# Performance work log

Measured on AMD Instinct MI355X. Metric: run time of the kernel, lower is better.

Reference implementation:

```python
import jax, jax.numpy as jnp
import numpy as np

N_GRAPHS = 256
N_NODES = 100000
N_EDGES = 1000000
EMB = 64
EMB_RBF = 16
NUM_HEADS = 1


def setup_inputs() -> dict:
    key = jax.random.key(0)
    ks = jax.random.split(key, 10)
    edge_emb = jax.random.normal(ks[0], (N_EDGES, EMB), dtype=jnp.float32)
    edge_index = jax.random.randint(ks[1], (2, N_EDGES), 0, N_NODES, dtype=jnp.int64)
    distance_vec = jax.random.normal(ks[2], (N_EDGES, 3), dtype=jnp.float32)
    lattice = jax.random.normal(ks[3], (N_GRAPHS, 3, 3), dtype=jnp.float32)
    batch = jnp.sort(jax.random.randint(ks[4], (N_NODES,), 0, N_GRAPHS, dtype=jnp.int64))
    rbf = jax.random.uniform(ks[5], (N_EDGES, EMB_RBF), dtype=jnp.float32)
    # Dense layers (GemNet Dense defaults to bias=False)
    s = 1.0 / np.sqrt(EMB)
    W1 = jax.random.normal(ks[6], (EMB, EMB), dtype=jnp.float32) * s
    W2 = jax.random.normal(ks[7], (EMB, EMB), dtype=jnp.float32) * s
    W_rbf = jax.random.normal(ks[8], (EMB_RBF, EMB), dtype=jnp.float32) * (1.0 / np.sqrt(EMB_RBF))
    W_out = jax.random.normal(ks[9], (EMB, NUM_HEADS), dtype=jnp.float32) * s
    return {"edge_emb": edge_emb, "edge_index": edge_index, "distance_vec": distance_vec,
            "lattice": lattice, "batch": batch, "rbf": rbf,
            "W1": W1, "W2": W2, "W_rbf": W_rbf, "W_out": W_out}


def reference(edge_emb, edge_index, distance_vec, lattice, batch, rbf, W1, W2, W_rbf, W_out):
    # compute_score_per_edge: MLP on edge embeddings, gated by RBF projection
    h = jax.nn.silu(edge_emb @ W1)            # [E, EMB]
    x_F = h @ W2                               # [E, EMB]
    x_F = x_F * (rbf @ W_rbf)                  # RBF gate, [E, EMB]
    edge_scores = x_F @ W_out                  # [E, num_heads]

    batch_edge = batch[edge_index[0]]          # graph id per edge, [E]
    # normalize_score=True: divide by edge count per graph
    num_edges = jax.ops.segment_sum(jnp.ones((edge_scores.shape[0],), dtype=edge_scores.dtype),
                                    batch_edge, num_segments=N_GRAPHS)
    edge_scores = edge_scores / num_edges[batch_edge, None]

    # edge_score_to_lattice_score_frac_symmetric, summed over heads (num_heads=1)
    s = edge_scores[:, 0]                      # [E]
    unit = distance_vec / jnp.linalg.norm(distance_vec, axis=-1, keepdims=True)
    outer = s[:, None, None] * unit[:, :, None] * distance_vec[:, None, :]  # [E,3,3]
    sym = 0.5 * (outer + jnp.swapaxes(outer, 1, 2))
    out = jax.ops.segment_sum(sym, batch_edge, num_segments=N_GRAPHS)       # [B,3,3]
    return out
```

## Files before the change

kernel.cpp:

```cpp
#include <hip/hip_runtime.h>
#include <math.h>

constexpr int G    = 256;
constexpr int EMB  = 64;
constexpr int ERBF = 16;

typedef __attribute__((ext_vector_type(8))) short bf16x8;
typedef __attribute__((ext_vector_type(4))) float f32x4;

static __device__ __forceinline__ short bf16_rne(float f) {
    union { float f; unsigned u; } v; v.f = f;
    unsigned r = (v.u + 0x7FFFu + ((v.u >> 16) & 1u)) >> 16;
    return (short)r;
}

__global__ void prep_M_kernel(const float* __restrict__ W2,
                              const float* __restrict__ W_rbf,
                              const float* __restrict__ W_out,
                              float* __restrict__ M) {
    int t = blockIdx.x * blockDim.x + threadIdx.x;
    if (t >= EMB * ERBF) return;
    int p = t >> 4;
    int k = t & 15;
    float acc = 0.f;
    for (int j = 0; j < EMB; ++j)
        acc = fmaf(W2[p * EMB + j] * W_out[j], W_rbf[k * EMB + j], acc);
    M[p * ERBF + k] = acc;
}

__global__ __launch_bounds__(256, 4) void edge_kernel(
    const float* __restrict__ edge_emb,
    const int*   __restrict__ edge_src,
    const float* __restrict__ dvec,
    const int*   __restrict__ batch,
    const float* __restrict__ rbf,
    const float* __restrict__ W1,
    const float* __restrict__ M,
    float* __restrict__ partial,
    int ne, int nblk)
{
    __shared__ float accs[G * 9];

    const int tid  = threadIdx.x;
    const int w    = tid >> 6;
    const int lane = tid & 63;
    const int q    = lane >> 4;
    const int col  = lane & 15;

    for (int i = tid; i < G * 9; i += 256) accs[i] = 0.f;

    bf16x8 w1f[4][2];
#pragma unroll
    for (int nt = 0; nt < 4; ++nt)
#pragma unroll
        for (int c = 0; c < 2; ++c) {
            bf16x8 wv;
#pragma unroll
            for (int j = 0; j < 8; ++j)
                wv[j] = bf16_rne(W1[(c * 32 + q * 8 + j) * EMB + nt * 16 + col]);
            w1f[nt][c] = wv;
        }
    bf16x8 mtf[4];
#pragma unroll
    for (int nt = 0; nt < 4; ++nt) {
        bf16x8 mv;
#pragma unroll
        for (int j = 0; j < 8; ++j) {
            int k = q * 8 + j;
            mv[j] = (k < ERBF) ? bf16_rne(M[(nt * 16 + col) * ERBF + k]) : (short)0;
        }
        mtf[nt] = mv;
    }
    __syncthreads();

    const long estep = (long)nblk * 4 * 16;
    for (long e0 = ((long)blockIdx.x * 4 + w) * 16; e0 < ne; e0 += estep) {
        const long erow  = e0 + col;
        const bool rowok = (erow < ne);

        bf16x8 af[2];
#pragma unroll
        for (int c = 0; c < 2; ++c) {
            bf16x8 a;
            if (rowok) {
                const float4* p = (const float4*)(edge_emb + (size_t)erow * EMB + c * 32 + q * 8);
                float4 v0 = p[0], v1 = p[1];
                a[0] = bf16_rne(v0.x); a[1] = bf16_rne(v0.y);
                a[2] = bf16_rne(v0.z); a[3] = bf16_rne(v0.w);
                a[4] = bf16_rne(v1.x); a[5] = bf16_rne(v1.y);
                a[6] = bf16_rne(v1.z); a[7] = bf16_rne(v1.w);
            } else {
#pragma unroll
                for (int j = 0; j < 8; ++j) a[j] = 0;
            }
            af[c] = a;
        }
        bf16x8 rf;
        if (q < 2 && rowok) {
            const float4* p = (const float4*)(rbf + (size_t)erow * ERBF + q * 8);
            float4 v0 = p[0], v1 = p[1];
            rf[0] = bf16_rne(v0.x); rf[1] = bf16_rne(v0.y);
            rf[2] = bf16_rne(v0.z); rf[3] = bf16_rne(v0.w);
            rf[4] = bf16_rne(v1.x); rf[5] = bf16_rne(v1.y);
            rf[6] = bf16_rne(v1.z); rf[7] = bf16_rne(v1.w);
        } else {
#pragma unroll
            for (int j = 0; j < 8; ++j) rf[j] = 0;
        }

        f32x4 hacc[4], vacc[4];
#pragma unroll
        for (int nt = 0; nt < 4; ++nt) {
            f32x4 z = {0.f, 0.f, 0.f, 0.f};
            z = __builtin_amdgcn_mfma_f32_16x16x32_bf16(af[0], w1f[nt][0], z, 0, 0, 0);
            z = __builtin_amdgcn_mfma_f32_16x16x32_bf16(af[1], w1f[nt][1], z, 0, 0, 0);
            hacc[nt] = z;
            f32x4 zv = {0.f, 0.f, 0.f, 0.f};
            vacc[nt] = __builtin_amdgcn_mfma_f32_16x16x32_bf16(rf, mtf[nt], zv, 0, 0, 0);
        }

        float sc[4];
#pragma unroll
        for (int r = 0; r < 4; ++r) {
            float acc = 0.f;
#pragma unroll
            for (int nt = 0; nt < 4; ++nt) {
                float x = hacc[nt][r];
                float s = x * __builtin_amdgcn_rcpf(1.f + __expf(-x));
                acc = fmaf(s, vacc[nt][r], acc);
            }
            sc[r] = acc;
        }
#pragma unroll
        for (int m = 1; m < 16; m <<= 1) {
#pragma unroll
            for (int r = 0; r < 4; ++r) sc[r] += __shfl_xor(sc[r], m);
        }

        if (col < 4) {
            long e = e0 + q * 4 + col;
            if (e < ne) {
                float s = sc[col];
                int   g = batch[edge_src[e]];
                size_t de = (size_t)e * 3;
                float dx = dvec[de], dy = dvec[de + 1], dz = dvec[de + 2];
                float nrm = sqrtf(dx * dx + dy * dy + dz * dz);
                float cc = s / nrm;
                float* a = &accs[g * 9];
                atomicAdd(a + 0, cc * dx * dx);
                atomicAdd(a + 1, cc * dx * dy);
                atomicAdd(a + 2, cc * dx * dz);
                atomicAdd(a + 3, cc * dy * dy);
                atomicAdd(a + 4, cc * dy * dz);
                atomicAdd(a + 5, cc * dz * dz);
                atomicAdd(a + 6, 1.0f);
            }
        }
    }

    __syncthreads();
    float* outp = partial + (size_t)blockIdx.x * (G * 8);
    {
        int g = tid;
        float* a = &accs[g * 9];
        float4 p0 = {a[0], a[1], a[2], a[3]};
        float4 p1 = {a[4], a[5], a[6], 0.f};
        ((float4*)(outp + g * 8))[0] = p0;
        ((float4*)(outp + g * 8))[1] = p1;
    }
}

__global__ __launch_bounds__(256) void reduce_kernel(
    const float* __restrict__ partial, float* __restrict__ out, int nblk)
{
    int g = blockIdx.x;
    __shared__ float red[256][8];
    float loc[8];
#pragma unroll
    for (int c = 0; c < 8; ++c) loc[c] = 0.f;

    for (int b = threadIdx.x; b < nblk; b += 256) {
        const float4* p = (const float4*)(partial + (size_t)b * (G * 8) + g * 8);
        float4 v0 = p[0], v1 = p[1];
        loc[0] += v0.x; loc[1] += v0.y; loc[2] += v0.z; loc[3] += v0.w;
        loc[4] += v1.x; loc[5] += v1.y; loc[6] += v1.z; loc[7] += v1.w;
    }
#pragma unroll
    for (int c = 0; c < 8; ++c) red[threadIdx.x][c] = loc[c];
    __syncthreads();

    for (int off = 128; off >= 1; off >>= 1) {
        if (threadIdx.x < off) {
#pragma unroll
            for (int c = 0; c < 8; ++c)
                red[threadIdx.x][c] += red[threadIdx.x + off][c];
        }
        __syncthreads();
    }

    if (threadIdx.x == 0) {
        float cnt = red[0][6];
        float inv = (cnt > 0.f) ? (1.f / cnt) : 0.f;
        float xx = red[0][0] * inv, xy = red[0][1] * inv, xz = red[0][2] * inv;
        float yy = red[0][3] * inv, yz = red[0][4] * inv, zz = red[0][5] * inv;
        float* o = out + g * 9;
        o[0] = xx; o[1] = xy; o[2] = xz;
        o[3] = xy; o[4] = yy; o[5] = yz;
        o[6] = xz; o[7] = yz; o[8] = zz;
    }
}

extern "C" void kernel_launch(void* const* d_in, const int* in_sizes, int n_in,
                              void* d_out, int out_size, void* d_ws, size_t ws_size,
                              hipStream_t stream) {
    const float* edge_emb   = (const float*)d_in[0];
    const int*   edge_index = (const int*)  d_in[1];
    const float* dvec       = (const float*)d_in[2];
    const int*   batch      = (const int*)  d_in[4];
    const float* rbf        = (const float*)d_in[5];
    const float* W1         = (const float*)d_in[6];
    const float* W2         = (const float*)d_in[7];
    const float* W_rbf      = (const float*)d_in[8];
    const float* W_out      = (const float*)d_in[9];
    float* out = (float*)d_out;

    int ne = in_sizes[0] / EMB;

    float* M = (float*)d_ws;
    float* partial = (float*)((char*)d_ws + 4096);
    size_t avail = (ws_size > 4096) ? (ws_size - 4096) : 0;
    int nblk = (int)(avail / (G * 8 * sizeof(float)));
    int tiles = (ne + 63) / 64;
    if (nblk > 1024)  nblk = 1024;
    if (nblk > tiles) nblk = tiles;
    if (nblk < 1)     nblk = 1;

    prep_M_kernel<<<4, 256, 0, stream>>>(W2, W_rbf, W_out, M);
    edge_kernel<<<nblk, 256, 0, stream>>>(edge_emb, edge_index, dvec, batch,
                                          rbf, W1, M, partial, ne, nblk);
    reduce_kernel<<<G, 256, 0, stream>>>(partial, out, nblk);
}
```

Measured before the change: 426.8 us.

## Software-pipeline edge tile loads with register double buffering and fewer blocks

Each wave now prefetches the next tile's edge embeddings, rbf, edge_src and distance vectors into registers while the current tile's MFMA and reduction work runs, so global load latency overlaps compute. Loads are clamped to the last edge instead of predicated, and the batch lookup is issued early. Launch bounds drop to 2 waves per SIMD to fit the extra registers, and the grid is capped at 512 blocks. This trades occupancy for latency hiding inside each wave, and there is a risk that lower occupancy hurts a bandwidth-bound kernel.

```diff
diff --git a/kernel.cpp b/kernel.cpp
--- a/kernel.cpp
+++ b/kernel.cpp
@@ -12,6 +12,14 @@
     union { float f; unsigned u; } v; v.f = f;
     unsigned r = (v.u + 0x7FFFu + ((v.u >> 16) & 1u)) >> 16;
     return (short)r;
+}
+static __device__ __forceinline__ bf16x8 cvt8(float4 a, float4 b) {
+    bf16x8 r;
+    r[0] = bf16_rne(a.x); r[1] = bf16_rne(a.y);
+    r[2] = bf16_rne(a.z); r[3] = bf16_rne(a.w);
+    r[4] = bf16_rne(b.x); r[5] = bf16_rne(b.y);
+    r[6] = bf16_rne(b.z); r[7] = bf16_rne(b.w);
+    return r;
 }
 
 __global__ void prep_M_kernel(const float* __restrict__ W2,
@@ -28,7 +36,38 @@
     M[p * ERBF + k] = acc;
 }
 
-__global__ __launch_bounds__(256, 4) void edge_kernel(
+struct Raw {
+    float4 a0, a1, a2, a3;
+    float4 r0, r1;
+    int    es;
+    float  dx, dy, dz;
+};
+
+static __device__ __forceinline__ Raw load_tile(
+    const float* __restrict__ edge_emb, const float* __restrict__ rbf,
+    const int* __restrict__ edge_src, const float* __restrict__ dvec,
+    long base, long nem1, int col, int q, int qq, bool owner, long eoff_own)
+{
+    Raw t;
+    long er = base + col; er = (er > nem1) ? nem1 : er;
+    const float* rowp = edge_emb + (size_t)er * EMB;
+    const float4* pa = (const float4*)(rowp + q * 8);
+    t.a0 = pa[0]; t.a1 = pa[1];
+    const float4* pb = (const float4*)(rowp + 32 + q * 8);
+    t.a2 = pb[0]; t.a3 = pb[1];
+    const float4* pr = (const float4*)(rbf + (size_t)er * ERBF + qq * 8);
+    t.r0 = pr[0]; t.r1 = pr[1];
+    t.es = 0; t.dx = 0.f; t.dy = 0.f; t.dz = 0.f;
+    if (owner) {
+        long eo = base + eoff_own; eo = (eo > nem1) ? nem1 : eo;
+        t.es = edge_src[eo];
+        size_t de = (size_t)eo * 3;
+        t.dx = dvec[de]; t.dy = dvec[de + 1]; t.dz = dvec[de + 2];
+    }
+    return t;
+}
+
+__global__ __launch_bounds__(256, 2) void edge_kernel(
     const float* __restrict__ edge_emb,
     const int*   __restrict__ edge_src,
     const float* __restrict__ dvec,
@@ -46,6 +85,9 @@
     const int lane = tid & 63;
     const int q    = lane >> 4;
     const int col  = lane & 15;
+    const int qq   = q & 1;
+    const bool owner = (col < 4);
+    const long eoff_own = q * 4 + col;
 
     for (int i = tid; i < G * 9; i += 256) accs[i] = 0.f;
 
@@ -73,37 +115,29 @@
     }
     __syncthreads();
 
-    const long estep = (long)nblk * 4 * 16;
-    for (long e0 = ((long)blockIdx.x * 4 + w) * 16; e0 < ne; e0 += estep) {
-        const long erow  = e0 + col;
-        const bool rowok = (erow < ne);
-
-        bf16x8 af[2];
-#pragma unroll
-        for (int c = 0; c < 2; ++c) {
-            bf16x8 a;
-            if (rowok) {
-                const float4* p = (const float4*)(edge_emb + (size_t)erow * EMB + c * 32 + q * 8);
-                float4 v0 = p[0], v1 = p[1];
-                a[0] = bf16_rne(v0.x); a[1] = bf16_rne(v0.y);
-                a[2] = bf16_rne(v0.z); a[3] = bf16_rne(v0.w);
-                a[4] = bf16_rne(v1.x); a[5] = bf16_rne(v1.y);
-                a[6] = bf16_rne(v1.z); a[7] = bf16_rne(v1.w);
-            } else {
-#pragma unroll
-                for (int j = 0; j < 8; ++j) a[j] = 0;
-            }
-            af[c] = a;
-        }
-        bf16x8 rf;
-        if (q < 2 && rowok) {
-            const float4* p = (const float4*)(rbf + (size_t)erow * ERBF + q * 8);
-            float4 v0 = p[0], v1 = p[1];
-            rf[0] = bf16_rne(v0.x); rf[1] = bf16_rne(v0.y);
-            rf[2] = bf16_rne(v0.z); rf[3] = bf16_rne(v0.w);
-            rf[4] = bf16_rne(v1.x); rf[5] = bf16_rne(v1.y);
-            rf[6] = bf16_rne(v1.z); rf[7] = bf16_rne(v1.w);
-        } else {
+    const long nem1  = (long)ne - 1;
+    const long estep = (long)nblk * 64;
+    long e0 = ((long)blockIdx.x * 4 + w) * 16;
+
+    Raw cur = load_tile(edge_emb, rbf, edge_src, dvec,
+                        (e0 <= nem1) ? e0 : nem1, nem1, col, q, qq, owner, eoff_own);
+
+    for (; e0 < ne; ) {
+        const long e1 = e0 + estep;
+        Raw nxt = load_tile(edge_emb, rbf, edge_src, dvec,
+                            (e1 <= nem1) ? e1 : e0, nem1, col, q, qq, owner, eoff_own);
+        int g = 0;
+        if (owner) g = batch[cur.es];
+
+        const bool rowok = (e0 + col) <= nem1;
+        bf16x8 af0 = cvt8(cur.a0, cur.a1);
+        bf16x8 af1 = cvt8(cur.a2, cur.a3);
+        bf16x8 rf  = cvt8(cur.r0, cur.r1);
+        if (!rowok) {
+#pragma unroll
+            for (int j = 0; j < 8; ++j) { af0[j] = 0; af1[j] = 0; }
+        }
+        if (q >= 2 || !rowok) {
 #pragma unroll
             for (int j = 0; j < 8; ++j) rf[j] = 0;
         }
@@ -112,8 +146,8 @@
 #pragma unroll
         for (int nt = 0; nt < 4; ++nt) {
             f32x4 z = {0.f, 0.f, 0.f, 0.f};
-            z = __builtin_amdgcn_mfma_f32_16x16x32_bf16(af[0], w1f[nt][0], z, 0, 0, 0);
-            z = __builtin_amdgcn_mfma_f32_16x16x32_bf16(af[1], w1f[nt][1], z, 0, 0, 0);
+            z = __builtin_amdgcn_mfma_f32_16x16x32_bf16(af0, w1f[nt][0], z, 0, 0, 0);
+            z = __builtin_amdgcn_mfma_f32_16x16x32_bf16(af1, w1f[nt][1], z, 0, 0, 0);
             hacc[nt] = z;
             f32x4 zv = {0.f, 0.f, 0.f, 0.f};
             vacc[nt] = __builtin_amdgcn_mfma_f32_16x16x32_bf16(rf, mtf[nt], zv, 0, 0, 0);
@@ -137,13 +171,11 @@
             for (int r = 0; r < 4; ++r) sc[r] += __shfl_xor(sc[r], m);
         }
 
-        if (col < 4) {
-            long e = e0 + q * 4 + col;
+        if (owner) {
+            long e = e0 + eoff_own;
             if (e < ne) {
-                float s = sc[col];
-                int   g = batch[edge_src[e]];
-                size_t de = (size_t)e * 3;
-                float dx = dvec[de], dy = dvec[de + 1], dz = dvec[de + 2];
+                float s  = sc[col];
+                float dx = cur.dx, dy = cur.dy, dz = cur.dz;
                 float nrm = sqrtf(dx * dx + dy * dy + dz * dz);
                 float cc = s / nrm;
                 float* a = &accs[g * 9];
@@ -156,17 +188,19 @@
                 atomicAdd(a + 6, 1.0f);
             }
         }
+        cur = nxt;
+        e0  = e1;
     }
 
     __syncthreads();
     float* outp = partial + (size_t)blockIdx.x * (G * 8);
     {
-        int g = tid;
-        float* a = &accs[g * 9];
+        int gg = tid;
+        float* a = &accs[gg * 9];
         float4 p0 = {a[0], a[1], a[2], a[3]};
         float4 p1 = {a[4], a[5], a[6], 0.f};
-        ((float4*)(outp + g * 8))[0] = p0;
-        ((float4*)(outp + g * 8))[1] = p1;
+        ((float4*)(outp + gg * 8))[0] = p0;
+        ((float4*)(outp + gg * 8))[1] = p1;
     }
 }
 
@@ -231,7 +265,7 @@
     size_t avail = (ws_size > 4096) ? (ws_size - 4096) : 0;
     int nblk = (int)(avail / (G * 8 * sizeof(float)));
     int tiles = (ne + 63) / 64;
-    if (nblk > 1024)  nblk = 1024;
+    if (nblk > 512)   nblk = 512;
     if (nblk > tiles) nblk = tiles;
     if (nblk < 1)     nblk = 1;
 
```

New measurement: 430.6 us. No clear change (+0.9%).

## Split edge kernel into MFMA score pass and separate scatter pass

Applied to the files above, without the earlier changes.

Splits the fused edge kernel in two. The first kernel computes per-edge scores with MFMA, two 16-row tiles per wave per iteration, with all loads issued before conversion and clamped rows instead of branches. It writes the scores to workspace. The second kernel reads the scores plus the gather and distance data at one edge per thread and does the shared-memory atomics. This aims to stop the serialized atomic and gather work from stalling the MFMA waves, at the cost of an extra score round trip through memory and an extra launch. It also assumes the workspace is large enough for the scores plus 512 partial blocks.

```diff
diff --git a/kernel.cpp b/kernel.cpp
--- a/kernel.cpp
+++ b/kernel.cpp
@@ -12,6 +12,14 @@
     union { float f; unsigned u; } v; v.f = f;
     unsigned r = (v.u + 0x7FFFu + ((v.u >> 16) & 1u)) >> 16;
     return (short)r;
+}
+static __device__ __forceinline__ bf16x8 cvt8(float4 a, float4 b) {
+    bf16x8 r;
+    r[0] = bf16_rne(a.x); r[1] = bf16_rne(a.y);
+    r[2] = bf16_rne(a.z); r[3] = bf16_rne(a.w);
+    r[4] = bf16_rne(b.x); r[5] = bf16_rne(b.y);
+    r[6] = bf16_rne(b.z); r[7] = bf16_rne(b.w);
+    return r;
 }
 
 __global__ void prep_M_kernel(const float* __restrict__ W2,
@@ -28,27 +36,20 @@
     M[p * ERBF + k] = acc;
 }
 
-__global__ __launch_bounds__(256, 4) void edge_kernel(
+__global__ __launch_bounds__(256, 2) void score_kernel(
     const float* __restrict__ edge_emb,
-    const int*   __restrict__ edge_src,
-    const float* __restrict__ dvec,
-    const int*   __restrict__ batch,
     const float* __restrict__ rbf,
     const float* __restrict__ W1,
     const float* __restrict__ M,
-    float* __restrict__ partial,
-    int ne, int nblk)
+    float* __restrict__ scores,
+    int ne)
 {
-    __shared__ float accs[G * 9];
-
     const int tid  = threadIdx.x;
     const int w    = tid >> 6;
     const int lane = tid & 63;
     const int q    = lane >> 4;
     const int col  = lane & 15;
 
-    for (int i = tid; i < G * 9; i += 256) accs[i] = 0.f;
-
     bf16x8 w1f[4][2];
 #pragma unroll
     for (int nt = 0; nt < 4; ++nt)
@@ -71,91 +72,112 @@
         }
         mtf[nt] = mv;
     }
+
+    const long nem1   = (long)ne - 1;
+    const long stride = (long)gridDim.x * 4 * 32;
+    for (long base = ((long)blockIdx.x * 4 + w) * 32; base < ne; base += stride) {
+        float4 a[2][4];
+        float4 rr[2][2];
+#pragma unroll
+        for (int st = 0; st < 2; ++st) {
+            long er = base + st * 16 + col;
+            if (er > nem1) er = nem1;
+            const float* rowp = edge_emb + (size_t)er * EMB;
+            const float4* pa = (const float4*)(rowp + q * 8);
+            a[st][0] = pa[0]; a[st][1] = pa[1];
+            const float4* pb = (const float4*)(rowp + 32 + q * 8);
+            a[st][2] = pb[0]; a[st][3] = pb[1];
+            if (q < 2) {
+                const float4* pr = (const float4*)(rbf + (size_t)er * ERBF + q * 8);
+                rr[st][0] = pr[0]; rr[st][1] = pr[1];
+            }
+        }
+
+        float sc[2][4];
+#pragma unroll
+        for (int st = 0; st < 2; ++st) {
+            bf16x8 af0 = cvt8(a[st][0], a[st][1]);
+            bf16x8 af1 = cvt8(a[st][2], a[st][3]);
+            bf16x8 rf;
+            if (q < 2) {
+                rf = cvt8(rr[st][0], rr[st][1]);
+            } else {
+#pragma unroll
+                for (int j = 0; j < 8; ++j) rf[j] = 0;
+            }
+
+            f32x4 hacc[4], vacc[4];
+#pragma unroll
+            for (int nt = 0; nt < 4; ++nt) {
+                f32x4 z = {0.f, 0.f, 0.f, 0.f};
+                z = __builtin_amdgcn_mfma_f32_16x16x32_bf16(af0, w1f[nt][0], z, 0, 0, 0);
+                z = __builtin_amdgcn_mfma_f32_16x16x32_bf16(af1, w1f[nt][1], z, 0, 0, 0);
+                hacc[nt] = z;
+                f32x4 zv = {0.f, 0.f, 0.f, 0.f};
+                vacc[nt] = __builtin_amdgcn_mfma_f32_16x16x32_bf16(rf, mtf[nt], zv, 0, 0, 0);
+            }
+
+#pragma unroll
+            for (int r = 0; r < 4; ++r) {
+                float acc = 0.f;
+#pragma unroll
+                for (int nt = 0; nt < 4; ++nt) {
+                    float x = hacc[nt][r];
+                    float s = x * __builtin_amdgcn_rcpf(1.f + __expf(-x));
+                    acc = fmaf(s, vacc[nt][r], acc);
+                }
+                sc[st][r] = acc;
+            }
+        }
+
+#pragma unroll
+        for (int m = 1; m < 16; m <<= 1) {
+#pragma unroll
+            for (int st = 0; st < 2; ++st)
+#pragma unroll
+                for (int r = 0; r < 4; ++r)
+                    sc[st][r] += __shfl_xor(sc[st][r], m);
+        }
+
+        if (col < 4) {
+#pragma unroll
+            for (int st = 0; st < 2; ++st) {
+                long e = base + st * 16 + q * 4 + col;
+                if (e < ne) scores[e] = sc[st][col];
+            }
+        }
+    }
+}
+
+__global__ __launch_bounds__(256) void scatter_kernel(
+    const float* __restrict__ scores,
+    const int*   __restrict__ edge_src,
+    const float* __restrict__ dvec,
+    const int*   __restrict__ batch,
+    float* __restrict__ partial,
+    int ne, int nblk)
+{
+    __shared__ float accs[G * 9];
+    const int tid = threadIdx.x;
+    for (int i = tid; i < G * 9; i += 256) accs[i] = 0.f;
     __syncthreads();
 
-    const long estep = (long)nblk * 4 * 16;
-    for (long e0 = ((long)blockIdx.x * 4 + w) * 16; e0 < ne; e0 += estep) {
-        const long erow  = e0 + col;
-        const bool rowok = (erow < ne);
-
-        bf16x8 af[2];
-#pragma unroll
-        for (int c = 0; c < 2; ++c) {
-            bf16x8 a;
-            if (rowok) {
-                const float4* p = (const float4*)(edge_emb + (size_t)erow * EMB + c * 32 + q * 8);
-                float4 v0 = p[0], v1 = p[1];
-                a[0] = bf16_rne(v0.x); a[1] = bf16_rne(v0.y);
-                a[2] = bf16_rne(v0.z); a[3] = bf16_rne(v0.w);
-                a[4] = bf16_rne(v1.x); a[5] = bf16_rne(v1.y);
-                a[6] = bf16_rne(v1.z); a[7] = bf16_rne(v1.w);
-            } else {
-#pragma unroll
-                for (int j = 0; j < 8; ++j) a[j] = 0;
-            }
-            af[c] = a;
-        }
-        bf16x8 rf;
-        if (q < 2 && rowok) {
-            const float4* p = (const float4*)(rbf + (size_t)erow * ERBF + q * 8);
-            float4 v0 = p[0], v1 = p[1];
-            rf[0] = bf16_rne(v0.x); rf[1] = bf16_rne(v0.y);
-            rf[2] = bf16_rne(v0.z); rf[3] = bf16_rne(v0.w);
-            rf[4] = bf16_rne(v1.x); rf[5] = bf16_rne(v1.y);
-            rf[6] = bf16_rne(v1.z); rf[7] = bf16_rne(v1.w);
-        } else {
-#pragma unroll
-            for (int j = 0; j < 8; ++j) rf[j] = 0;
-        }
-
-        f32x4 hacc[4], vacc[4];
-#pragma unroll
-        for (int nt = 0; nt < 4; ++nt) {
-            f32x4 z = {0.f, 0.f, 0.f, 0.f};
-            z = __builtin_amdgcn_mfma_f32_16x16x32_bf16(af[0], w1f[nt][0], z, 0, 0, 0);
-            z = __builtin_amdgcn_mfma_f32_16x16x32_bf16(af[1], w1f[nt][1], z, 0, 0, 0);
-            hacc[nt] = z;
-            f32x4 zv = {0.f, 0.f, 0.f, 0.f};
-            vacc[nt] = __builtin_amdgcn_mfma_f32_16x16x32_bf16(rf, mtf[nt], zv, 0, 0, 0);
-        }
-
-        float sc[4];
-#pragma unroll
-        for (int r = 0; r < 4; ++r) {
-            float acc = 0.f;
-#pragma unroll
-            for (int nt = 0; nt < 4; ++nt) {
-                float x = hacc[nt][r];
-                float s = x * __builtin_amdgcn_rcpf(1.f + __expf(-x));
-                acc = fmaf(s, vacc[nt][r], acc);
-            }
-            sc[r] = acc;
-        }
-#pragma unroll
-        for (int m = 1; m < 16; m <<= 1) {
-#pragma unroll
-            for (int r = 0; r < 4; ++r) sc[r] += __shfl_xor(sc[r], m);
-        }
-
-        if (col < 4) {
-            long e = e0 + q * 4 + col;
-            if (e < ne) {
-                float s = sc[col];
-                int   g = batch[edge_src[e]];
-                size_t de = (size_t)e * 3;
-                float dx = dvec[de], dy = dvec[de + 1], dz = dvec[de + 2];
-                float nrm = sqrtf(dx * dx + dy * dy + dz * dz);
-                float cc = s / nrm;
-                float* a = &accs[g * 9];
-                atomicAdd(a + 0, cc * dx * dx);
-                atomicAdd(a + 1, cc * dx * dy);
-                atomicAdd(a + 2, cc * dx * dz);
-                atomicAdd(a + 3, cc * dy * dy);
-                atomicAdd(a + 4, cc * dy * dz);
-                atomicAdd(a + 5, cc * dz * dz);
-                atomicAdd(a + 6, 1.0f);
-            }
-        }
+    const long estep = (long)nblk * 256;
+    for (long e = (long)blockIdx.x * 256 + tid; e < ne; e += estep) {
+        float s  = scores[e];
+        int   g  = batch[edge_src[e]];
+        size_t de = (size_t)e * 3;
+        float dx = dvec[de], dy = dvec[de + 1], dz = dvec[de + 2];
+        float nrm = sqrtf(dx * dx + dy * dy + dz * dz);
+        float cc  = s / nrm;
+        float* a = &accs[g * 9];
+        atomicAdd(a + 0, cc * dx * dx);
+        atomicAdd(a + 1, cc * dx * dy);
+        atomicAdd(a + 2, cc * dx * dz);
+        atomicAdd(a + 3, cc * dy * dy);
+        atomicAdd(a + 4, cc * dy * dz);
+        atomicAdd(a + 5, cc * dz * dz);
+        atomicAdd(a + 6, 1.0f);
     }
 
     __syncthreads();
@@ -227,16 +249,16 @@
     int ne = in_sizes[0] / EMB;
 
     float* M = (float*)d_ws;
-    float* partial = (float*)((char*)d_ws + 4096);
-    size_t avail = (ws_size > 4096) ? (ws_size - 4096) : 0;
-    int nblk = (int)(avail / (G * 8 * sizeof(float)));
-    int tiles = (ne + 63) / 64;
-    if (nblk > 1024)  nblk = 1024;
-    if (nblk > tiles) nblk = tiles;
-    if (nblk < 1)     nblk = 1;
+    float* scores = (float*)((char*)d_ws + 4096);
+    size_t score_bytes = (((size_t)ne * 4) + 255) & ~(size_t)255;
+    float* partial = (float*)((char*)d_ws + 4096 + score_bytes);
+
+    const int SA = 512;
+    const int NB = 512;
 
     prep_M_kernel<<<4, 256, 0, stream>>>(W2, W_rbf, W_out, M);
-    edge_kernel<<<nblk, 256, 0, stream>>>(edge_emb, edge_index, dvec, batch,
-                                          rbf, W1, M, partial, ne, nblk);
-    reduce_kernel<<<G, 256, 0, stream>>>(partial, out, nblk);
-}
+    score_kernel<<<SA, 256, 0, stream>>>(edge_emb, rbf, W1, M, scores, ne);
+    scatter_kernel<<<NB, 256, 0, stream>>>(scores, edge_index, dvec, batch,
+                                           partial, ne, NB);
+    reduce_kernel<<<G, 256, 0, stream>>>(partial, out, NB);
+}
```

Result: slower. 456.4 us (+6.9%).
